# Kernel tuning notes

Measured on AMD Instinct MI355X. Metric: run time of the kernel, lower is better.

The kernel has to match this reference:

```python
import jax, jax.numpy as jnp
import numpy as np

B, S, D, H, FF = 4, 1024, 1024, 16, 4096
HD = D // H
SCALE = float(np.sqrt(HD))
LAMBDA_MIN = 0.5
LAMBDA_MAX = 0.5
EPS = 1e-5


def _layernorm(x, g, b):
    mu = jnp.mean(x, axis=-1, keepdims=True)
    var = jnp.mean(jnp.square(x - mu), axis=-1, keepdims=True)
    return (x - mu) * jax.lax.rsqrt(var + EPS) * g + b


def _qbnn_layer(h, W, bW, J, lam_base, g, be):
    # s_prev = tanh(h); h_tilde = h W + b; delta_j = (sum_i s_prev_i J_ij) * tanh(h_tilde)_j
    s_prev = jnp.tanh(h)
    h_tilde = h @ W + bW
    s_raw = jnp.tanh(h_tilde)
    delta = (s_prev @ J) * s_raw
    lam_n = jax.nn.sigmoid(lam_base)
    dynamic_factor = 0.5  # eval mode, call_count=0 -> 0.5+0.5*sin(0)
    lam_eff = LAMBDA_MIN + (LAMBDA_MAX - LAMBDA_MIN) * (lam_n * 0.7 + dynamic_factor * 0.3)
    h_hat = h_tilde + lam_eff * delta
    return jax.nn.gelu(_layernorm(h_hat, g, be), approximate=False)


def setup_inputs() -> dict:
    key = jax.random.key(0)
    ks = jax.random.split(key, 24)
    f32 = jnp.float32
    lin = lambda k, i, o: jax.random.normal(k, (i, o), f32) / np.sqrt(i)
    inp = {
        'x': jax.random.normal(ks[0], (B, S, D), f32),
        # attention projections (stored as [in, out]; y = x @ W + b)
        'wq': lin(ks[1], D, D), 'bq': jnp.zeros((D,), f32),
        'wk': lin(ks[2], D, D), 'bk': jnp.zeros((D,), f32),
        'wv': lin(ks[3], D, D), 'bv': jnp.zeros((D,), f32),
        'wo': lin(ks[4], D, D), 'bo': jnp.zeros((D,), f32),
        'J_attn': jax.random.normal(ks[5], (H, HD, HD), f32) * 0.02,
        'lambda_attn': jnp.asarray(0.5, f32),
        'g_attn': jnp.ones((D,), f32), 'b_attn': jnp.zeros((D,), f32),
        # ffn layer 1 (D -> FF)
        'W1': lin(ks[6], D, FF), 'b1': jnp.zeros((FF,), f32),
        'J1': jax.random.normal(ks[7], (D, FF), f32) * 0.02,
        'lam1': jnp.asarray(0.5, f32),
        'g1': jnp.ones((FF,), f32), 'be1': jnp.zeros((FF,), f32),
        # ffn layer 2 (FF -> D)
        'W2': lin(ks[8], FF, D), 'b2': jnp.zeros((D,), f32),
        'J2': jax.random.normal(ks[9], (FF, D), f32) * 0.02,
        'lam2': jnp.asarray(0.5, f32),
        'g2': jnp.ones((D,), f32), 'be2': jnp.zeros((D,), f32),
        # ffn pre-norm
        'g_ffn': jnp.ones((D,), f32), 'b_ffn': jnp.zeros((D,), f32),
    }
    return inp


def reference(x, wq, bq, wk, bk, wv, bv, wo, bo, J_attn, lambda_attn, g_attn, b_attn,
              W1, b1, J1, lam1, g1, be1, W2, b2, J2, lam2, g2, be2, g_ffn, b_ffn):
    # --- attention (pre-norm) ---
    xn = _layernorm(x, g_attn, b_attn)
    split = lambda t: t.reshape(B, S, H, HD).transpose(0, 2, 1, 3)  # bshd -> bhsd
    Q = split(xn @ wq + bq)
    K = split(xn @ wk + bk)
    V = split(xn @ wv + bv)
    scores = jnp.einsum('bhid,bhjd->bhij', Q, K) / SCALE
    tQJ = jnp.einsum('bhid,hde->bhie', jnp.tanh(Q), J_attn)
    delta = jnp.einsum('bhie,bhje->bhij', tQJ, jnp.tanh(K))
    probs = jax.nn.softmax(scores + lambda_attn * delta, axis=-1)
    attn = jnp.einsum('bhij,bhjd->bhid', probs, V)
    attn = attn.transpose(0, 2, 1, 3).reshape(B, S, D) @ wo + bo
    x = x + attn
    # --- QBNN FFN (pre-norm) ---
    h = _layernorm(x, g_ffn, b_ffn)
    h = _qbnn_layer(h, W1, b1, J1, lam1, g1, be1)
    h = _qbnn_layer(h, W2, b2, J2, lam2, g2, be2)
    return x + h
```

## Files before the change

kernel.cpp:

```cpp
#include <hip/hip_runtime.h>
#include <cmath>

typedef unsigned short u16;
typedef unsigned int   u32;
typedef short bhalf8 __attribute__((ext_vector_type(8)));
typedef float fx4    __attribute__((ext_vector_type(4)));

#define B_   4
#define S_   1024
#define D_   1024
#define H_   16
#define HD_  64
#define FF_  4096
#define NTOK (B_*S_)
#define QKVW 3072

__device__ __forceinline__ float b2f(u16 u) {
    u32 x = ((u32)u) << 16;
    return __uint_as_float(x);
}
__device__ __forceinline__ u16 f2b(float f) {
    u32 u = __float_as_uint(f);
    u32 r = (u + 0x7fffu + ((u >> 16) & 1u)) >> 16;
    return (u16)r;
}
__device__ __forceinline__ float ftanh(float x) {
    float e = __expf(2.f * x);
    return 1.f - 2.f / (e + 1.f);
}

#define GLDS16(g, l) __builtin_amdgcn_global_load_lds( \
    (const __attribute__((address_space(1))) void*)(g), \
    (__attribute__((address_space(3))) void*)(l), 16, 0, 0)

template <int N> __device__ __forceinline__ void waitvm() {
    if constexpr (N == 8) asm volatile("s_waitcnt vmcnt(8)" ::: "memory");
    else if constexpr (N == 6) asm volatile("s_waitcnt vmcnt(6)" ::: "memory");
    else if constexpr (N == 4) asm volatile("s_waitcnt vmcnt(4)" ::: "memory");
    else if constexpr (N == 3) asm volatile("s_waitcnt vmcnt(3)" ::: "memory");
    else if constexpr (N == 2) asm volatile("s_waitcnt vmcnt(2)" ::: "memory");
    else asm volatile("s_waitcnt vmcnt(0)" ::: "memory");
}

__device__ __forceinline__ void tile_swz(int gx, int gy, int& bx, int& by) {
    int bid = blockIdx.x;
    int nwg = gx * gy;
    if (((nwg | gy) & 7) == 0) {
        int chunk = nwg >> 3;
        int wg = (bid & 7) * chunk + (bid >> 3);
        int tps = gx << 3;
        int sup = wg / tps, rem = wg % tps;
        bx = rem >> 3;
        by = (sup << 3) + (rem & 7);
    } else {
        bx = bid % gx; by = bid / gx;
    }
}

__global__ __launch_bounds__(256) void cvt_t_k(const float* __restrict__ w0, const float* __restrict__ w1,
                                               const float* __restrict__ w2, const float* __restrict__ w3,
                                               const float* __restrict__ W1p, const float* __restrict__ J1p,
                                               const float* __restrict__ W2p, const float* __restrict__ J2p,
                                               u16* __restrict__ dst) {
    __shared__ u16 L[64][65];
    int bid = blockIdx.x, tid = threadIdx.x;
    const float* src; size_t dbase; int Kd, Nd, tk, tn;
    if (bid < 1024)      { int m = bid >> 8, t = bid & 255;
                           src = m == 0 ? w0 : m == 1 ? w1 : m == 2 ? w2 : w3;
                           dbase = (size_t)m << 20; Kd = 1024; Nd = 1024; tk = t >> 4; tn = t & 15; }
    else if (bid < 2048) { int t = bid - 1024; src = W1p; dbase = (size_t)4  << 20; Kd = 1024; Nd = 4096; tk = t >> 6; tn = t & 63; }
    else if (bid < 3072) { int t = bid - 2048; src = J1p; dbase = (size_t)8  << 20; Kd = 1024; Nd = 4096; tk = t >> 6; tn = t & 63; }
    else if (bid < 4096) { int t = bid - 3072; src = W2p; dbase = (size_t)12 << 20; Kd = 4096; Nd = 1024; tk = t >> 4; tn = t & 15; }
    else                 { int t = bid - 4096; src = J2p; dbase = (size_t)16 << 20; Kd = 4096; Nd = 1024; tk = t >> 4; tn = t & 15; }
    int k0 = tk * 64, n0 = tn * 64;
    int r = tid >> 2, c4 = (tid & 3) * 16;
    #pragma unroll
    for (int p = 0; p < 4; ++p) {
        float4 v = *(const float4*)&src[(size_t)(k0 + r) * Nd + n0 + c4 + p * 4];
        L[r][c4 + p * 4 + 0] = f2b(v.x);
        L[r][c4 + p * 4 + 1] = f2b(v.y);
        L[r][c4 + p * 4 + 2] = f2b(v.z);
        L[r][c4 + p * 4 + 3] = f2b(v.w);
    }
    __syncthreads();
    u16 o[16];
    #pragma unroll
    for (int j = 0; j < 16; ++j) o[j] = L[c4 + j][r];
    *(uint4*)&dst[dbase + (size_t)(n0 + r) * Kd + k0 + c4]     = *(uint4*)&o[0];
    *(uint4*)&dst[dbase + (size_t)(n0 + r) * Kd + k0 + c4 + 8] = *(uint4*)&o[8];
}

__global__ __launch_bounds__(256) void tanh_k(const u16* __restrict__ in, u16* __restrict__ outb) {
    size_t idx = ((size_t)blockIdx.x * 256 + threadIdx.x) * 8;
    uint4 v = *(const uint4*)&in[idx];
    const u16* p = (const u16*)&v;
    u16 o[8];
    #pragma unroll
    for (int j = 0; j < 8; ++j) o[j] = f2b(ftanh(b2f(p[j])));
    *(uint4*)&outb[idx] = *(uint4*)o;
}

template <int BM, int BN, int WM, int WN, int EPI, bool SEG>
__global__ __launch_bounds__(512, 2) void gemmP(const u16* __restrict__ A,
                                                const u16* __restrict__ Bt,
                                                const float* __restrict__ bA,
                                                const float* __restrict__ bB,
                                                const float* __restrict__ bC,
                                                const float* __restrict__ resid,
                                                void* __restrict__ Cout,
                                                int M, int N, int K) {
    constexpr int IA = BM / 128;
    constexpr int IB = BN / 128;
    constexpr int NWN = BN / WN;
    constexpr int FM = WM / 16, FN = WN / 16;
    __shared__ u16 As[4][BM * 32];
    __shared__ u16 Bs[4][BN * 32];

    const int tid = threadIdx.x;
    const int w = tid >> 6, ln = tid & 63;
    const int q = ln >> 4, mr = ln & 15;
    const int wmi = w / NWN, wni = w % NWN;
    int bx, by;
    tile_swz(N / BN, M / BM, bx, by);
    const int m0 = by * BM, n0 = bx * BN;

    const int lr = ln >> 2;
    const int sc = 8 * ((ln & 3) ^ ((ln >> 3) & 3));
    const int qx8 = 8 * (q ^ ((mr >> 1) & 3));

    const u16* aA[IA];
    const u16* aB[IB];
    #pragma unroll
    for (int i = 0; i < IA; ++i)
        aA[i] = A + (size_t)(m0 + 16 * (w + 8 * i) + lr) * K + sc;
    #pragma unroll
    for (int i = 0; i < IB; ++i)
        aB[i] = Bt + (size_t)(n0 + 16 * (w + 8 * i) + lr) * K + sc;

    fx4 acc[FM][FN];
    #pragma unroll
    for (int i = 0; i < FM; ++i)
        #pragma unroll
        for (int j = 0; j < FN; ++j) acc[i][j] = (fx4){0.f, 0.f, 0.f, 0.f};

#define GP_STAGE(slot, kk) do { \
        _Pragma("unroll") \
        for (int i = 0; i < IA; ++i) GLDS16(aA[i] + (kk), &As[slot][(16 * (w + 8 * i)) * 32]); \
        _Pragma("unroll") \
        for (int i = 0; i < IB; ++i) GLDS16(aB[i] + (kk), &Bs[slot][(16 * (w + 8 * i)) * 32]); \
    } while (0)

    const int NT = K >> 5;
    GP_STAGE(0, 0);
    GP_STAGE(1, 32);
    for (int t = 0; t < NT; ++t) {
        if (t + 2 < NT) {
            GP_STAGE((t + 2) & 3, (t + 2) << 5);
            waitvm<2 * (IA + IB)>();
        } else if (t + 1 < NT) {
            waitvm<IA + IB>();
        } else {
            waitvm<0>();
        }
        asm volatile("s_waitcnt lgkmcnt(0)" ::: "memory");
        __builtin_amdgcn_sched_barrier(0);
        __builtin_amdgcn_s_barrier();
        __builtin_amdgcn_sched_barrier(0);

        const int sl = t & 3;
        bhalf8 afr[FM], bfr[FN];
        const u16* Ap = &As[sl][0];
        const u16* Bp = &Bs[sl][0];
        #pragma unroll
        for (int fm = 0; fm < FM; ++fm)
            afr[fm] = *(const bhalf8*)&Ap[(wmi * WM + fm * 16 + mr) * 32 + qx8];
        #pragma unroll
        for (int fn = 0; fn < FN; ++fn)
            bfr[fn] = *(const bhalf8*)&Bp[(wni * WN + fn * 16 + mr) * 32 + qx8];

        __builtin_amdgcn_s_setprio(1);
        #pragma unroll
        for (int fm = 0; fm < FM; ++fm)
            #pragma unroll
            for (int fn = 0; fn < FN; ++fn)
                acc[fm][fn] = __builtin_amdgcn_mfma_f32_16x16x32_bf16(afr[fm], bfr[fn], acc[fm][fn], 0, 0, 0);
        __builtin_amdgcn_s_setprio(0);
    }
#undef GP_STAGE

    #pragma unroll
    for (int fn = 0; fn < FN; ++fn) {
        int col = n0 + wni * WN + fn * 16 + mr;
        float bs;
        if (SEG) {
            const float* bp = col < 1024 ? bA : (col < 2048 ? bB : bC);
            bs = bp[col & 1023];
        } else {
            bs = bA ? bA[col] : 0.f;
        }
        #pragma unroll
        for (int fm = 0; fm < FM; ++fm) {
            #pragma unroll
            for (int r = 0; r < 4; ++r) {
                int row    = m0 + wmi * WM + fm * 16 + q * 4 + r;
                size_t idx = (size_t)row * N + col;
                float v    = acc[fm][fn][r] + bs;
                if (EPI == 0) {
                    ((u16*)Cout)[idx] = f2b(v);
                } else if (EPI == 1) {
                    ((float*)Cout)[idx] = v + resid[idx];
                } else {
                    float ht = b2f(((u16*)Cout)[idx]);
                    ((u16*)Cout)[idx] = f2b(ht + 0.5f * v * ftanh(ht));
                }
            }
        }
    }
}

__global__ __launch_bounds__(256) void ln_k(const float* __restrict__ xin,
                                            const float* __restrict__ g,
                                            const float* __restrict__ bb,
                                            u16* __restrict__ out, int W) {
    __shared__ float red[8], red2[8], stats[2];
    int row = blockIdx.x, tid = threadIdx.x;
    float s = 0.f, ss = 0.f;
    for (int c = tid; c < W; c += 256) {
        float v = xin[(size_t)row * W + c];
        s += v; ss += v * v;
    }
    #pragma unroll
    for (int off = 32; off; off >>= 1) { s += __shfl_xor(s, off); ss += __shfl_xor(ss, off); }
    int wave = tid >> 6, lane = tid & 63;
    if (lane == 0) { red[wave] = s; red2[wave] = ss; }
    __syncthreads();
    if (tid == 0) {
        float S = 0.f, SS = 0.f;
        for (int w2 = 0; w2 < 4; ++w2) { S += red[w2]; SS += red2[w2]; }
        float mu = S / W;
        stats[0] = mu;
        stats[1] = rsqrtf(SS / W - mu * mu + 1e-5f);
    }
    __syncthreads();
    float mu = stats[0], rs = stats[1];
    for (int c = tid; c < W; c += 256)
        out[(size_t)row * W + c] = f2b((xin[(size_t)row * W + c] - mu) * rs * g[c] + bb[c]);
}

template <bool RES, bool OUT_F32>
__global__ __launch_bounds__(256) void lngelu_k(const u16* __restrict__ u,
                                                const float* __restrict__ g,
                                                const float* __restrict__ be,
                                                const float* __restrict__ resid,
                                                void* __restrict__ out, int W) {
    __shared__ float ub[4096];
    __shared__ float red[8], red2[8], stats[2];
    int row = blockIdx.x, tid = threadIdx.x;
    float s = 0.f, ss = 0.f;
    for (int c = tid; c < W; c += 256) {
        float v = b2f(u[(size_t)row * W + c]);
        ub[c] = v; s += v; ss += v * v;
    }
    #pragma unroll
    for (int off = 32; off; off >>= 1) { s += __shfl_xor(s, off); ss += __shfl_xor(ss, off); }
    int wave = tid >> 6, lane = tid & 63;
    if (lane == 0) { red[wave] = s; red2[wave] = ss; }
    __syncthreads();
    if (tid == 0) {
        float S = 0.f, SS = 0.f;
        for (int w2 = 0; w2 < 4; ++w2) { S += red[w2]; SS += red2[w2]; }
        float mu = S / W;
        stats[0] = mu;
        stats[1] = rsqrtf(SS / W - mu * mu + 1e-5f);
    }
    __syncthreads();
    float mu = stats[0], rs = stats[1];
    for (int c = tid; c < W; c += 256) {
        float v = (ub[c] - mu) * rs * g[c] + be[c];
        float y = 0.5f * v * (1.f + erff(v * 0.70710678118654752f));
        if (RES) y += resid[(size_t)row * W + c];
        if (OUT_F32) ((float*)out)[(size_t)row * W + c] = y;
        else         ((u16*)out)[(size_t)row * W + c] = f2b(y);
    }
}

__global__ __launch_bounds__(256) void aug_q_k(const u16* __restrict__ QKV,
                                               const float* __restrict__ J,
                                               const float* __restrict__ lamp,
                                               u16* __restrict__ QA) {
    __shared__ float Jl[64][68];
    __shared__ float Tq[64][65];
    int blk = blockIdx.x;
    int bh = blk >> 4, st = blk & 15;
    int b = bh >> 4, h = bh & 15;
    int s0 = st * 64;
    int tid = threadIdx.x;
    float lam = lamp[0];

    for (int i = tid; i < 4096; i += 256)
        Jl[i >> 6][i & 63] = J[h * 4096 + i];
    for (int i = tid; i < 4096; i += 256) {
        int r = i >> 6, c = i & 63;
        float v  = b2f(QKV[(size_t)(b * S_ + s0 + r) * QKVW + h * 64 + c]);
        Tq[r][c] = ftanh(v);
        QA[((size_t)(bh * S_ + s0 + r)) * 128 + c] = f2b(v * 0.125f);
    }
    __syncthreads();

    int r = tid >> 2, c0 = (tid & 3) * 16;
    float acc[16];
    #pragma unroll
    for (int j = 0; j < 16; ++j) acc[j] = 0.f;
    for (int k = 0; k < 64; ++k) {
        float a = Tq[r][k];
        #pragma unroll
        for (int j4 = 0; j4 < 4; ++j4) {
            float4 jv = *(const float4*)&Jl[k][c0 + j4 * 4];
            acc[j4 * 4 + 0] += a * jv.x;
            acc[j4 * 4 + 1] += a * jv.y;
            acc[j4 * 4 + 2] += a * jv.z;
            acc[j4 * 4 + 3] += a * jv.w;
        }
    }
    size_t orow = ((size_t)(bh * S_ + s0 + r)) * 128 + 64 + c0;
    #pragma unroll
    for (int j = 0; j < 16; ++j) QA[orow + j] = f2b(lam * acc[j]);
}

__global__ __launch_bounds__(256) void aug_k_k(const u16* __restrict__ QKV,
                                               u16* __restrict__ KA) {
    int idx = blockIdx.x * 256 + threadIdx.x;
    int d = idx & (D_ - 1);
    int bs = idx >> 10;
    int h = d >> 6, hd = d & 63;
    int b = bs >> 10, si = bs & (S_ - 1);
    u16 v      = QKV[(size_t)bs * QKVW + 1024 + d];
    size_t row = (size_t)((b * H_ + h) * S_ + si);
    KA[row * 128 + hd]      = v;
    KA[row * 128 + 64 + hd] = f2b(ftanh(b2f(v)));
}

__global__ __launch_bounds__(256) void vt_k(const u16* __restrict__ QKV,
                                            u16* __restrict__ VT) {
    __shared__ u16 L[64][72];
    int blk = blockIdx.x;
    int bh = blk >> 4, st = blk & 15;
    int b = bh >> 4, h = bh & 15;
    int s0 = st * 64;
    int tid = threadIdx.x;
    #pragma unroll
    for (int p = 0; p < 2; ++p) {
        int i = p * 2048 + tid * 8;
        int r = i >> 6, c = i & 63;
        uint4 v = *(const uint4*)&QKV[((size_t)(b * S_ + s0 + r)) * QKVW + 2048 + h * 64 + c];
        *(uint4*)&L[r][c] = v;
    }
    __syncthreads();
    #pragma unroll
    for (int p = 0; p < 2; ++p) {
        int i = p * 2048 + tid * 8;
        int d = i >> 6, s = i & 63;
        u16 o[8];
        #pragma unroll
        for (int j = 0; j < 8; ++j) o[j] = L[s + j][d];
        *(uint4*)&VT[((size_t)(bh * 64 + d)) * S_ + s0 + s] = *(uint4*)o;
    }
}

#define QS_STRIDE 136
#define PS_STRIDE 72
__global__ __launch_bounds__(256) void attn_k(const u16* __restrict__ QA,
                                              const u16* __restrict__ KA,
                                              const u16* __restrict__ VT,
                                              u16* __restrict__ out) {
    __shared__ u16 Qs[64 * QS_STRIDE];
    __shared__ u16 Ks[2][64 * 128];
    __shared__ u16 Vs[2][64 * 64];
    __shared__ u16 Ps[64 * PS_STRIDE];

    const int tid  = threadIdx.x;
    const int w    = tid >> 6, lane = tid & 63;
    const int q    = lane >> 4, mr = lane & 15;
    const int bh   = blockIdx.x >> 4;
    const int qt   = blockIdx.x & 15;

    #pragma unroll
    for (int p = 0; p < 4; ++p) {
        int idx = p * 2048 + tid * 8;
        int row = idx >> 7, col = idx & 127;
        uint4 v4 = *(const uint4*)&QA[((size_t)(bh * S_ + qt * 64 + row)) * 128 + col];
        *(uint4*)&Qs[row * QS_STRIDE + col] = v4;
    }

#define STAGEKV(pp, kt) do { \
        _Pragma("unroll") \
        for (int i = 0; i < 4; ++i) { \
            int R = w * 16 + i * 4 + (lane >> 4); \
            GLDS16(KA + ((size_t)(bh * S_ + (kt) * 64 + R)) * 128 + 8 * ((lane & 15) ^ (R & 7)), \
                   &Ks[pp][(w * 16 + i * 4) * 128]); \
        } \
        _Pragma("unroll") \
        for (int i = 0; i < 2; ++i) { \
            int Rv = w * 16 + i * 8 + (lane >> 3); \
            GLDS16(VT + ((size_t)(bh * 64 + Rv)) * S_ + (kt) * 64 + 8 * ((lane & 7) ^ (Rv & 7)), \
                   &Vs[pp][(w * 16 + i * 8) * 64]); \
        } \
    } while (0)

    STAGEKV(0, 0);
    __syncthreads();

    bhalf8 afr[4];
    #pragma unroll
    for (int ks = 0; ks < 4; ++ks)
        afr[ks] = *(const bhalf8*)&Qs[(w * 16 + mr) * QS_STRIDE + ks * 32 + q * 8];

    fx4 zero = {0.f, 0.f, 0.f, 0.f};
    fx4 O[4] = {zero, zero, zero, zero};
    float m[4]  = {-3e38f, -3e38f, -3e38f, -3e38f};
    float l[4]  = {0.f, 0.f, 0.f, 0.f};

    int p = 0;
    for (int kt = 0; kt < 16; ++kt) {
        if (kt + 1 < 16) {
            STAGEKV(p ^ 1, kt + 1);
            waitvm<6>();
        } else {
            waitvm<0>();
        }
        __builtin_amdgcn_sched_barrier(0);
        __builtin_amdgcn_s_barrier();
        __builtin_amdgcn_sched_barrier(0);

        fx4 St[4] = {zero, zero, zero, zero};
        __builtin_amdgcn_s_setprio(1);
        #pragma unroll
        for (int nt = 0; nt < 4; ++nt) {
            #pragma unroll
            for (int ks = 0; ks < 4; ++ks) {
                bhalf8 bf = *(const bhalf8*)&Ks[p][(nt * 16 + mr) * 128 + 8 * (((ks * 4 + q) ^ (mr & 7)))];
                St[nt] = __builtin_amdgcn_mfma_f32_16x16x32_bf16(afr[ks], bf, St[nt], 0, 0, 0);
            }
        }
        __builtin_amdgcn_s_setprio(0);

        float alpha[4];
        #pragma unroll
        for (int r = 0; r < 4; ++r) {
            float mx = fmaxf(fmaxf(St[0][r], St[1][r]), fmaxf(St[2][r], St[3][r]));
            #pragma unroll
            for (int off = 8; off; off >>= 1) mx = fmaxf(mx, __shfl_xor(mx, off));
            float nm = fmaxf(m[r], mx);
            alpha[r] = __expf(m[r] - nm);
            m[r] = nm;
            float ps = 0.f;
            #pragma unroll
            for (int nt = 0; nt < 4; ++nt) {
                float pv = __expf(St[nt][r] - nm);
                St[nt][r] = pv;
                ps += pv;
            }
            #pragma unroll
            for (int off = 8; off; off >>= 1) ps += __shfl_xor(ps, off);
            l[r] = l[r] * alpha[r] + ps;
        }
        #pragma unroll
        for (int nt = 0; nt < 4; ++nt) {
            #pragma unroll
            for (int r = 0; r < 4; ++r) {
                Ps[(w * 16 + q * 4 + r) * PS_STRIDE + nt * 16 + mr] = f2b(St[nt][r]);
                O[nt][r] *= alpha[r];
            }
        }

        __builtin_amdgcn_s_setprio(1);
        #pragma unroll
        for (int ks = 0; ks < 2; ++ks) {
            bhalf8 pa = *(const bhalf8*)&Ps[(w * 16 + mr) * PS_STRIDE + ks * 32 + q * 8];
            #pragma unroll
            for (int nt = 0; nt < 4; ++nt) {
                bhalf8 bf = *(const bhalf8*)&Vs[p][(nt * 16 + mr) * 64 + 8 * (((ks * 4 + q) ^ (mr & 7)))];
                O[nt] = __builtin_amdgcn_mfma_f32_16x16x32_bf16(pa, bf, O[nt], 0, 0, 0);
            }
        }
        __builtin_amdgcn_s_setprio(0);
        asm volatile("s_waitcnt lgkmcnt(0)" ::: "memory");
        __builtin_amdgcn_sched_barrier(0);
        __builtin_amdgcn_s_barrier();
        p ^= 1;
    }
#undef STAGEKV

    const int b = bh >> 4, h = bh & 15;
    #pragma unroll
    for (int nt = 0; nt < 4; ++nt) {
        int d = nt * 16 + mr;
        #pragma unroll
        for (int r = 0; r < 4; ++r) {
            int row = qt * 64 + w * 16 + q * 4 + r;
            out[((size_t)(b * S_ + row)) * D_ + h * 64 + d] = f2b(O[nt][r] / l[r]);
        }
    }
}

extern "C" void kernel_launch(void* const* d_in, const int* in_sizes, int n_in,
                              void* d_out, int out_size, void* d_ws, size_t ws_size,
                              hipStream_t stream) {
    const float* x      = (const float*)d_in[0];
    const float* wq     = (const float*)d_in[1];
    const float* bq     = (const float*)d_in[2];
    const float* wk     = (const float*)d_in[3];
    const float* bk     = (const float*)d_in[4];
    const float* wv     = (const float*)d_in[5];
    const float* bv     = (const float*)d_in[6];
    const float* wo     = (const float*)d_in[7];
    const float* bo     = (const float*)d_in[8];
    const float* Jattn  = (const float*)d_in[9];
    const float* lamA   = (const float*)d_in[10];
    const float* g_attn = (const float*)d_in[11];
    const float* b_attn = (const float*)d_in[12];
    const float* W1     = (const float*)d_in[13];
    const float* b1     = (const float*)d_in[14];
    const float* J1     = (const float*)d_in[15];
    const float* g1     = (const float*)d_in[17];
    const float* be1    = (const float*)d_in[18];
    const float* W2     = (const float*)d_in[19];
    const float* b2     = (const float*)d_in[20];
    const float* J2     = (const float*)d_in[21];
    const float* g2     = (const float*)d_in[23];
    const float* be2    = (const float*)d_in[24];
    const float* g_ffn  = (const float*)d_in[25];
    const float* b_ffn  = (const float*)d_in[26];
    float* out = (float*)d_out;
    (void)in_sizes; (void)n_in; (void)out_size; (void)ws_size;

    char* wsp = (char*)d_ws;
    const size_t MB = 1u << 20;
    u16* WB = (u16*)(wsp);
    const u16* qkvT = WB;
    const u16* woT  = WB + ((size_t)3 << 20);
    const u16* W1T  = WB + ((size_t)4 << 20);
    const u16* J1T  = WB + ((size_t)8 << 20);
    const u16* W2T  = WB + ((size_t)12 << 20);
    const u16* J2T  = WB + ((size_t)16 << 20);
    u16*   XN   = (u16*)(wsp + 40 * MB);
    u16*   AT   = (u16*)(wsp + 40 * MB);
    u16*   U2   = (u16*)(wsp + 40 * MB);
    u16*   QKVb = (u16*)(wsp + 48 * MB);
    u16*   Hb   = (u16*)(wsp + 48 * MB);
    float* X2   = (float*)(wsp + 56 * MB);
    u16*   QA   = (u16*)(wsp + 72 * MB);
    u16*   KA   = (u16*)(wsp + 88 * MB);
    u16*   U1   = (u16*)(wsp + 72 * MB);
    u16*   VT   = (u16*)(wsp + 104 * MB);

    dim3 blk(256), blk5(512);
    cvt_t_k<<<5120, blk, 0, stream>>>(wq, wk, wv, wo, W1, J1, W2, J2, WB);
    ln_k<<<NTOK, blk, 0, stream>>>(x, g_attn, b_attn, XN, D_);
    gemmP<128, 128, 64, 32, 0, true><<<(QKVW / 128) * (NTOK / 128), blk5, 0, stream>>>(
        XN, qkvT, bq, bk, bv, nullptr, QKVb, NTOK, QKVW, D_);
    aug_q_k<<<B_ * H_ * (S_ / 64), blk, 0, stream>>>(QKVb, Jattn, lamA, QA);
    aug_k_k<<<(NTOK * D_) / 256, blk, 0, stream>>>(QKVb, KA);
    vt_k<<<B_ * H_ * (S_ / 64), blk, 0, stream>>>(QKVb, VT);
    attn_k<<<B_ * H_ * (S_ / 64), blk, 0, stream>>>(QA, KA, VT, AT);
    gemmP<128, 128, 64, 32, 1, false><<<(D_ / 128) * (NTOK / 128), blk5, 0, stream>>>(
        AT, woT, bo, nullptr, nullptr, x, X2, NTOK, D_, D_);
    ln_k<<<NTOK, blk, 0, stream>>>(X2, g_ffn, b_ffn, Hb, D_);
    gemmP<128, 128, 64, 32, 0, false><<<(FF_ / 128) * (NTOK / 128), blk5, 0, stream>>>(
        Hb, W1T, b1, nullptr, nullptr, nullptr, U1, NTOK, FF_, D_);
    tanh_k<<<(NTOK * D_) / 2048, blk, 0, stream>>>(Hb, Hb);
    gemmP<128, 128, 64, 32, 2, false><<<(FF_ / 128) * (NTOK / 128), blk5, 0, stream>>>(
        Hb, J1T, nullptr, nullptr, nullptr, nullptr, U1, NTOK, FF_, D_);
    lngelu_k<false, false><<<NTOK, blk, 0, stream>>>(U1, g1, be1, nullptr, U1, FF_);
    gemmP<128, 128, 64, 32, 0, false><<<(D_ / 128) * (NTOK / 128), blk5, 0, stream>>>(
        U1, W2T, b2, nullptr, nullptr, nullptr, U2, NTOK, D_, FF_);
    tanh_k<<<(NTOK * FF_) / 2048, blk, 0, stream>>>(U1, U1);
    gemmP<128, 128, 64, 32, 2, false><<<(D_ / 128) * (NTOK / 128), blk5, 0, stream>>>(
        U1, J2T, nullptr, nullptr, nullptr, nullptr, U2, NTOK, D_, FF_);
    lngelu_k<true, true><<<NTOK, blk, 0, stream>>>(U2, g2, be2, X2, out, D_);
}
```

Baseline: 656.8 us.

## Fuse paired W/J GEMMs into dual-GEMM kernel and use lazy exp2 softmax rescaling

Adds a dual GEMM kernel that computes h@W and tanh(h)@J in one pass over a shared output tile and applies the combine epilogue directly. The tanh of the input is now produced by the preceding layernorm kernels instead of a separate tanh pass. This removes extra launches, a second read-modify-write of the output, and redundant loads. Attention softmax switches to exp2 with a log2e prescale and skips rescaling the running output unless the max grows by more than a threshold. The second FFN layer takes the dual path only when the workspace is large enough, and the dual kernel uses more LDS per block.

```diff
diff --git a/kernel.cpp b/kernel.cpp
--- a/kernel.cpp
+++ b/kernel.cpp
@@ -14,6 +14,7 @@
 #define FF_  4096
 #define NTOK (B_*S_)
 #define QKVW 3072
+#define LOG2E 1.44269504088896f
 
 __device__ __forceinline__ float b2f(u16 u) {
     u32 x = ((u32)u) << 16;
@@ -28,6 +29,11 @@
     float e = __expf(2.f * x);
     return 1.f - 2.f / (e + 1.f);
 }
+__device__ __forceinline__ float fexp2(float x) {
+    float r;
+    asm("v_exp_f32 %0, %1" : "=v"(r) : "v"(x));
+    return r;
+}
 
 #define GLDS16(g, l) __builtin_amdgcn_global_load_lds( \
     (const __attribute__((address_space(1))) void*)(g), \
@@ -37,7 +43,6 @@
     if constexpr (N == 8) asm volatile("s_waitcnt vmcnt(8)" ::: "memory");
     else if constexpr (N == 6) asm volatile("s_waitcnt vmcnt(6)" ::: "memory");
     else if constexpr (N == 4) asm volatile("s_waitcnt vmcnt(4)" ::: "memory");
-    else if constexpr (N == 3) asm volatile("s_waitcnt vmcnt(3)" ::: "memory");
     else if constexpr (N == 2) asm volatile("s_waitcnt vmcnt(2)" ::: "memory");
     else asm volatile("s_waitcnt vmcnt(0)" ::: "memory");
 }
@@ -218,10 +223,116 @@
     }
 }
 
+__global__ __launch_bounds__(512) void dgemmP(const u16* __restrict__ A,
+                                              const u16* __restrict__ At,
+                                              const u16* __restrict__ WT,
+                                              const u16* __restrict__ JT,
+                                              const float* __restrict__ bias,
+                                              u16* __restrict__ Cout,
+                                              int M, int N, int K) {
+    __shared__ u16 As[4][128 * 32];
+    __shared__ u16 Ts[4][128 * 32];
+    __shared__ u16 Ws[4][128 * 32];
+    __shared__ u16 Js[4][128 * 32];
+
+    const int tid = threadIdx.x;
+    const int w = tid >> 6, ln = tid & 63;
+    const int q = ln >> 4, mr = ln & 15;
+    const int wmi = w >> 2, wni = w & 3;
+    int bx, by;
+    tile_swz(N >> 7, M >> 7, bx, by);
+    const int m0 = by * 128, n0 = bx * 128;
+
+    const int lr = ln >> 2;
+    const int sc = 8 * ((ln & 3) ^ ((ln >> 3) & 3));
+    const int qx8 = 8 * (q ^ ((mr >> 1) & 3));
+
+    const u16* aA = A  + (size_t)(m0 + 16 * w + lr) * K + sc;
+    const u16* aT = At + (size_t)(m0 + 16 * w + lr) * K + sc;
+    const u16* aW = WT + (size_t)(n0 + 16 * w + lr) * K + sc;
+    const u16* aJ = JT + (size_t)(n0 + 16 * w + lr) * K + sc;
+
+    fx4 aw[4][2], aj[4][2];
+    #pragma unroll
+    for (int i = 0; i < 4; ++i)
+        #pragma unroll
+        for (int j = 0; j < 2; ++j) {
+            aw[i][j] = (fx4){0.f, 0.f, 0.f, 0.f};
+            aj[i][j] = (fx4){0.f, 0.f, 0.f, 0.f};
+        }
+
+#define DG_STAGE(slot, kk) do { \
+        GLDS16(aA + (kk), &As[slot][(16 * w) * 32]); \
+        GLDS16(aT + (kk), &Ts[slot][(16 * w) * 32]); \
+        GLDS16(aW + (kk), &Ws[slot][(16 * w) * 32]); \
+        GLDS16(aJ + (kk), &Js[slot][(16 * w) * 32]); \
+    } while (0)
+
+    const int NT = K >> 5;
+    DG_STAGE(0, 0);
+    DG_STAGE(1, 32);
+    for (int t = 0; t < NT; ++t) {
+        if (t + 2 < NT) {
+            DG_STAGE((t + 2) & 3, (t + 2) << 5);
+            waitvm<8>();
+        } else if (t + 1 < NT) {
+            waitvm<4>();
+        } else {
+            waitvm<0>();
+        }
+        asm volatile("s_waitcnt lgkmcnt(0)" ::: "memory");
+        __builtin_amdgcn_sched_barrier(0);
+        __builtin_amdgcn_s_barrier();
+        __builtin_amdgcn_sched_barrier(0);
+
+        const int sl = t & 3;
+        bhalf8 afr[4], tfr[4], bwf[2], bjf[2];
+        #pragma unroll
+        for (int fm = 0; fm < 4; ++fm) {
+            afr[fm] = *(const bhalf8*)&As[sl][(wmi * 64 + fm * 16 + mr) * 32 + qx8];
+            tfr[fm] = *(const bhalf8*)&Ts[sl][(wmi * 64 + fm * 16 + mr) * 32 + qx8];
+        }
+        #pragma unroll
+        for (int fn = 0; fn < 2; ++fn) {
+            bwf[fn] = *(const bhalf8*)&Ws[sl][(wni * 32 + fn * 16 + mr) * 32 + qx8];
+            bjf[fn] = *(const bhalf8*)&Js[sl][(wni * 32 + fn * 16 + mr) * 32 + qx8];
+        }
+
+        __builtin_amdgcn_s_setprio(1);
+        #pragma unroll
+        for (int fm = 0; fm < 4; ++fm)
+            #pragma unroll
+            for (int fn = 0; fn < 2; ++fn) {
+                aw[fm][fn] = __builtin_amdgcn_mfma_f32_16x16x32_bf16(afr[fm], bwf[fn], aw[fm][fn], 0, 0, 0);
+                aj[fm][fn] = __builtin_amdgcn_mfma_f32_16x16x32_bf16(tfr[fm], bjf[fn], aj[fm][fn], 0, 0, 0);
+            }
+        __builtin_amdgcn_s_setprio(0);
+    }
+#undef DG_STAGE
+
+    #pragma unroll
+    for (int fn = 0; fn < 2; ++fn) {
+        int col = n0 + wni * 32 + fn * 16 + mr;
+        float bs = bias[col];
+        #pragma unroll
+        for (int fm = 0; fm < 4; ++fm) {
+            #pragma unroll
+            for (int r = 0; r < 4; ++r) {
+                int row    = m0 + wmi * 64 + fm * 16 + q * 4 + r;
+                size_t idx = (size_t)row * N + col;
+                float ht   = aw[fm][fn][r] + bs;
+                Cout[idx]  = f2b(ht + 0.5f * aj[fm][fn][r] * ftanh(ht));
+            }
+        }
+    }
+}
+
+template <bool WT>
 __global__ __launch_bounds__(256) void ln_k(const float* __restrict__ xin,
                                             const float* __restrict__ g,
                                             const float* __restrict__ bb,
-                                            u16* __restrict__ out, int W) {
+                                            u16* __restrict__ out,
+                                            u16* __restrict__ tout, int W) {
     __shared__ float red[8], red2[8], stats[2];
     int row = blockIdx.x, tid = threadIdx.x;
     float s = 0.f, ss = 0.f;
@@ -243,16 +354,20 @@
     }
     __syncthreads();
     float mu = stats[0], rs = stats[1];
-    for (int c = tid; c < W; c += 256)
-        out[(size_t)row * W + c] = f2b((xin[(size_t)row * W + c] - mu) * rs * g[c] + bb[c]);
-}
-
-template <bool RES, bool OUT_F32>
+    for (int c = tid; c < W; c += 256) {
+        float v = (xin[(size_t)row * W + c] - mu) * rs * g[c] + bb[c];
+        out[(size_t)row * W + c] = f2b(v);
+        if (WT) tout[(size_t)row * W + c] = f2b(ftanh(v));
+    }
+}
+
+template <bool RES, bool OUT_F32, bool WT>
 __global__ __launch_bounds__(256) void lngelu_k(const u16* __restrict__ u,
                                                 const float* __restrict__ g,
                                                 const float* __restrict__ be,
                                                 const float* __restrict__ resid,
-                                                void* __restrict__ out, int W) {
+                                                void* __restrict__ out,
+                                                u16* __restrict__ tout, int W) {
     __shared__ float ub[4096];
     __shared__ float red[8], red2[8], stats[2];
     int row = blockIdx.x, tid = threadIdx.x;
@@ -281,6 +396,7 @@
         if (RES) y += resid[(size_t)row * W + c];
         if (OUT_F32) ((float*)out)[(size_t)row * W + c] = y;
         else         ((u16*)out)[(size_t)row * W + c] = f2b(y);
+        if (WT) tout[(size_t)row * W + c] = f2b(ftanh(y));
     }
 }
 
@@ -295,7 +411,7 @@
     int b = bh >> 4, h = bh & 15;
     int s0 = st * 64;
     int tid = threadIdx.x;
-    float lam = lamp[0];
+    float lam = lamp[0] * LOG2E;
 
     for (int i = tid; i < 4096; i += 256)
         Jl[i >> 6][i & 63] = J[h * 4096 + i];
@@ -303,7 +419,7 @@
         int r = i >> 6, c = i & 63;
         float v  = b2f(QKV[(size_t)(b * S_ + s0 + r) * QKVW + h * 64 + c]);
         Tq[r][c] = ftanh(v);
-        QA[((size_t)(bh * S_ + s0 + r)) * 128 + c] = f2b(v * 0.125f);
+        QA[((size_t)(bh * S_ + s0 + r)) * 128 + c] = f2b(v * (0.125f * LOG2E));
     }
     __syncthreads();
 
@@ -444,34 +560,45 @@
         }
         __builtin_amdgcn_s_setprio(0);
 
-        float alpha[4];
+        float mx[4];
+        float gmx = -3e38f;
         #pragma unroll
         for (int r = 0; r < 4; ++r) {
-            float mx = fmaxf(fmaxf(St[0][r], St[1][r]), fmaxf(St[2][r], St[3][r]));
-            #pragma unroll
-            for (int off = 8; off; off >>= 1) mx = fmaxf(mx, __shfl_xor(mx, off));
-            float nm = fmaxf(m[r], mx);
-            alpha[r] = __expf(m[r] - nm);
-            m[r] = nm;
+            float v = fmaxf(fmaxf(St[0][r], St[1][r]), fmaxf(St[2][r], St[3][r]));
+            #pragma unroll
+            for (int off = 8; off; off >>= 1) v = fmaxf(v, __shfl_xor(v, off));
+            mx[r] = v;
+            gmx = fmaxf(gmx, v - m[r]);
+        }
+        if (!__all(gmx <= 8.f)) {
+            #pragma unroll
+            for (int r = 0; r < 4; ++r) {
+                float nm = fmaxf(m[r], mx[r]);
+                float alpha = fexp2(m[r] - nm);
+                m[r] = nm;
+                l[r] *= alpha;
+                #pragma unroll
+                for (int nt = 0; nt < 4; ++nt) O[nt][r] *= alpha;
+            }
+        }
+        #pragma unroll
+        for (int r = 0; r < 4; ++r) {
             float ps = 0.f;
             #pragma unroll
             for (int nt = 0; nt < 4; ++nt) {
-                float pv = __expf(St[nt][r] - nm);
+                float pv = fexp2(St[nt][r] - m[r]);
                 St[nt][r] = pv;
                 ps += pv;
             }
             #pragma unroll
             for (int off = 8; off; off >>= 1) ps += __shfl_xor(ps, off);
-            l[r] = l[r] * alpha[r] + ps;
-        }
-        #pragma unroll
-        for (int nt = 0; nt < 4; ++nt) {
-            #pragma unroll
-            for (int r = 0; r < 4; ++r) {
+            l[r] += ps;
+        }
+        #pragma unroll
+        for (int nt = 0; nt < 4; ++nt)
+            #pragma unroll
+            for (int r = 0; r < 4; ++r)
                 Ps[(w * 16 + q * 4 + r) * PS_STRIDE + nt * 16 + mr] = f2b(St[nt][r]);
-                O[nt][r] *= alpha[r];
-            }
-        }
 
         __builtin_amdgcn_s_setprio(1);
         #pragma unroll
@@ -532,7 +659,7 @@
     const float* g_ffn  = (const float*)d_in[25];
     const float* b_ffn  = (const float*)d_in[26];
     float* out = (float*)d_out;
-    (void)in_sizes; (void)n_in; (void)out_size; (void)ws_size;
+    (void)in_sizes; (void)n_in; (void)out_size;
 
     char* wsp = (char*)d_ws;
     const size_t MB = 1u << 20;
@@ -545,6 +672,7 @@
     const u16* J2T  = WB + ((size_t)16 << 20);
     u16*   XN   = (u16*)(wsp + 40 * MB);
     u16*   AT   = (u16*)(wsp + 40 * MB);
+    u16*   Ht1  = (u16*)(wsp + 40 * MB);
     u16*   U2   = (u16*)(wsp + 40 * MB);
     u16*   QKVb = (u16*)(wsp + 48 * MB);
     u16*   Hb   = (u16*)(wsp + 48 * MB);
@@ -553,10 +681,12 @@
     u16*   KA   = (u16*)(wsp + 88 * MB);
     u16*   U1   = (u16*)(wsp + 72 * MB);
     u16*   VT   = (u16*)(wsp + 104 * MB);
+    u16*   Ht2  = (u16*)(wsp + 104 * MB);
+    const bool dual2 = ws_size >= 136 * MB;
 
     dim3 blk(256), blk5(512);
     cvt_t_k<<<5120, blk, 0, stream>>>(wq, wk, wv, wo, W1, J1, W2, J2, WB);
-    ln_k<<<NTOK, blk, 0, stream>>>(x, g_attn, b_attn, XN, D_);
+    ln_k<false><<<NTOK, blk, 0, stream>>>(x, g_attn, b_attn, XN, nullptr, D_);
     gemmP<128, 128, 64, 32, 0, true><<<(QKVW / 128) * (NTOK / 128), blk5, 0, stream>>>(
         XN, qkvT, bq, bk, bv, nullptr, QKVb, NTOK, QKVW, D_);
     aug_q_k<<<B_ * H_ * (S_ / 64), blk, 0, stream>>>(QKVb, Jattn, lamA, QA);
@@ -565,17 +695,20 @@
     attn_k<<<B_ * H_ * (S_ / 64), blk, 0, stream>>>(QA, KA, VT, AT);
     gemmP<128, 128, 64, 32, 1, false><<<(D_ / 128) * (NTOK / 128), blk5, 0, stream>>>(
         AT, woT, bo, nullptr, nullptr, x, X2, NTOK, D_, D_);
-    ln_k<<<NTOK, blk, 0, stream>>>(X2, g_ffn, b_ffn, Hb, D_);
-    gemmP<128, 128, 64, 32, 0, false><<<(FF_ / 128) * (NTOK / 128), blk5, 0, stream>>>(
-        Hb, W1T, b1, nullptr, nullptr, nullptr, U1, NTOK, FF_, D_);
-    tanh_k<<<(NTOK * D_) / 2048, blk, 0, stream>>>(Hb, Hb);
-    gemmP<128, 128, 64, 32, 2, false><<<(FF_ / 128) * (NTOK / 128), blk5, 0, stream>>>(
-        Hb, J1T, nullptr, nullptr, nullptr, nullptr, U1, NTOK, FF_, D_);
-    lngelu_k<false, false><<<NTOK, blk, 0, stream>>>(U1, g1, be1, nullptr, U1, FF_);
-    gemmP<128, 128, 64, 32, 0, false><<<(D_ / 128) * (NTOK / 128), blk5, 0, stream>>>(
-        U1, W2T, b2, nullptr, nullptr, nullptr, U2, NTOK, D_, FF_);
-    tanh_k<<<(NTOK * FF_) / 2048, blk, 0, stream>>>(U1, U1);
-    gemmP<128, 128, 64, 32, 2, false><<<(D_ / 128) * (NTOK / 128), blk5, 0, stream>>>(
-        U1, J2T, nullptr, nullptr, nullptr, nullptr, U2, NTOK, D_, FF_);
-    lngelu_k<true, true><<<NTOK, blk, 0, stream>>>(U2, g2, be2, X2, out, D_);
-}
+    ln_k<true><<<NTOK, blk, 0, stream>>>(X2, g_ffn, b_ffn, Hb, Ht1, D_);
+    dgemmP<<<(FF_ / 128) * (NTOK / 128), blk5, 0, stream>>>(
+        Hb, Ht1, W1T, J1T, b1, U1, NTOK, FF_, D_);
+    if (dual2) {
+        lngelu_k<false, false, true><<<NTOK, blk, 0, stream>>>(U1, g1, be1, nullptr, U1, Ht2, FF_);
+        dgemmP<<<(D_ / 128) * (NTOK / 128), blk5, 0, stream>>>(
+            U1, Ht2, W2T, J2T, b2, U2, NTOK, D_, FF_);
+    } else {
+        lngelu_k<false, false, false><<<NTOK, blk, 0, stream>>>(U1, g1, be1, nullptr, U1, nullptr, FF_);
+        gemmP<128, 128, 64, 32, 0, false><<<(D_ / 128) * (NTOK / 128), blk5, 0, stream>>>(
+            U1, W2T, b2, nullptr, nullptr, nullptr, U2, NTOK, D_, FF_);
+        tanh_k<<<(NTOK * FF_) / 2048, blk, 0, stream>>>(U1, U1);
+        gemmP<128, 128, 64, 32, 2, false><<<(D_ / 128) * (NTOK / 128), blk5, 0, stream>>>(
+            U1, J2T, nullptr, nullptr, nullptr, nullptr, U2, NTOK, D_, FF_);
+    }
+    lngelu_k<true, true, false><<<NTOK, blk, 0, stream>>>(U2, g2, be2, X2, out, nullptr, D_);
+}
```

Result: faster. 613.0 us (-6.7%).
